# Optimization experiments

Measured on AMD Instinct MI355X. Metric: run time of the kernel, lower is better.

## Reference

```python
import jax, jax.numpy as jnp
import numpy as np
from math import log2, ceil

HEADS, DIM_HEAD, BLOCK, EPS = 16, 64, 16, 1e-8


def setup_inputs() -> dict:
    key = jax.random.key(0)
    k1, k2, k3, k4 = jax.random.split(key, 4)
    b, n, dim = 4, 4096, 1024
    inner = HEADS * DIM_HEAD
    return {
        "x": jax.random.normal(k1, (b, n, dim), jnp.float32),
        "w_qkv": jax.random.normal(k2, (inner * 3, dim), jnp.float32) * 0.02,
        "w_out": jax.random.normal(k3, (dim, inner), jnp.float32) * 0.02,
        "b_out": jax.random.normal(k4, (dim,), jnp.float32) * 0.02,
    }


def reference(x, w_qkv, w_out, b_out):
    b, n, dim = x.shape
    pad_to_len = 2 ** ceil(log2(n))
    if pad_to_len != n:
        x = jnp.pad(x, ((0, 0), (0, pad_to_len - n), (0, 0)))
    qkv = x @ w_qkv.T  # torch Linear (no bias): weight is [out, in]
    q, k, v = jnp.split(qkv, 3, axis=-1)

    def split_heads(t):
        return t.reshape(b, pad_to_len, HEADS, DIM_HEAD).transpose(0, 2, 1, 3).reshape(b * HEADS, pad_to_len, DIM_HEAD)

    q = split_heads(q) * DIM_HEAD ** -0.5
    k = split_heads(k)
    v = split_heads(v)

    num_levels = int(log2(pad_to_len // BLOCK)) - 1
    # hierarchical coarsening: q,k averaged over pairs, v summed over pairs
    qkvs = [(q, k, v)]
    for _ in range(num_levels):
        q = q.reshape(q.shape[0], -1, 2, DIM_HEAD).mean(2)
        k = k.reshape(k.shape[0], -1, 2, DIM_HEAD).mean(2)
        v = v.reshape(v.shape[0], -1, 2, DIM_HEAD).sum(2)
        qkvs.append((q, k, v))

    neg_max = -jnp.finfo(x.dtype).max
    idx = jnp.arange(pad_to_len)
    Ysum = jnp.zeros((b * HEADS, pad_to_len, DIM_HEAD), x.dtype)
    Asum = jnp.zeros((b * HEADS, pad_to_len), x.dtype)

    for lvl, (ql, kl, vl) in enumerate(qkvs):
        B = ql.shape[0]
        nb = ql.shape[1] // BLOCK  # number of blocks at this level
        ql = ql.reshape(B, nb, BLOCK, DIM_HEAD)
        kl = kl.reshape(B, nb, BLOCK, DIM_HEAD)
        vl = vl.reshape(B, nb, BLOCK, DIM_HEAD)
        if lvl == 0:
            # finest level: causal diagonal block attention
            S = jnp.einsum('bnid,bnjd->bnij', ql, kl)
            S = jnp.where(jnp.triu(jnp.ones((BLOCK, BLOCK), bool), 1), neg_max, S)
            S = S - S.max(-1, keepdims=True)
            A = jnp.exp(S)
            y = jnp.einsum('bnij,bnjd->bnid', A, vl).reshape(B, pad_to_len, DIM_HEAD)
            Av = A.sum(-1).reshape(B, pad_to_len)
        else:
            # off-diagonal: second block of each pair attends to first block of pair
            q2 = ql.reshape(B, nb // 2, 2, BLOCK, DIM_HEAD)[:, :, 1]
            k1b = kl.reshape(B, nb // 2, 2, BLOCK, DIM_HEAD)[:, :, 0]  # flip_every_two then take [:,1]
            v1b = vl.reshape(B, nb // 2, 2, BLOCK, DIM_HEAD)[:, :, 0]
            S = jnp.einsum('bnid,bnjd->bnij', q2, k1b)
            S = S - S.max(-1, keepdims=True)
            A = jnp.exp(S)
            y = jnp.einsum('bnij,bnjd->bnid', A, v1b)  # [B, nb/2, BLOCK, d]
            Av = A.sum(-1)
            # zero-pad first block of each pair, flatten blocks back to sequence
            y = jnp.pad(y[:, :, None], ((0, 0), (0, 0), (1, 0), (0, 0), (0, 0))).reshape(B, -1, DIM_HEAD)
            Av = jnp.pad(Av[:, :, None], ((0, 0), (0, 0), (1, 0), (0, 0))).reshape(B, -1)
            # expand coarsened positions to full resolution (consecutive repeats)
            y = jnp.repeat(y, 2 ** lvl, axis=1)
            Av = jnp.repeat(Av, 2 ** lvl, axis=1)
        # causal keep-mask: max original index inside the coarsened key group <= query index
        seq_key = (idx >> lvl << lvl) + (2 ** lvl - 1)
        keep = seq_key <= idx  # at lvl=0 seq_key == idx -> keep all
        Ysum = Ysum + jnp.where(keep[None, :, None], y, 0.0)
        Asum = Asum + jnp.where(keep[None, :], Av, 0.0)

    out = Ysum / (Asum + EPS)[..., None]
    out = out.reshape(b, HEADS, pad_to_len, DIM_HEAD).transpose(0, 2, 1, 3).reshape(b, pad_to_len, HEADS * DIM_HEAD)
    out = out @ w_out.T + b_out
    return out[:, :n]
```

## Files before the change

### kernel.cpp

```cpp
#include <hip/hip_runtime.h>

typedef __bf16 bf16_t;
typedef __attribute__((ext_vector_type(8))) __bf16 bf16x8;
typedef __attribute__((ext_vector_type(4))) float f32x4;

#define MFMA(a,b,c) __builtin_amdgcn_mfma_f32_16x16x32_bf16(a,b,c,0,0,0)

static __device__ __forceinline__ unsigned short f2bfbits(float f){
  unsigned int u = __builtin_bit_cast(unsigned int, f);
  return (unsigned short)((u + 0x7FFFu + ((u >> 16) & 1u)) >> 16);
}
static __device__ __forceinline__ float bits2f(unsigned int b){
  return __builtin_bit_cast(float, b << 16);
}
static __device__ __forceinline__ void gl_lds16(const void* g, void* l){
  __builtin_amdgcn_global_load_lds(
      (const __attribute__((address_space(1))) void*)(g),
      (__attribute__((address_space(3))) void*)(l), 16, 0, 0);
}
static __device__ __forceinline__ void unpack8(uint4 raw, float* f){
  f[0]=bits2f(raw.x&0xFFFFu); f[1]=bits2f(raw.x>>16);
  f[2]=bits2f(raw.y&0xFFFFu); f[3]=bits2f(raw.y>>16);
  f[4]=bits2f(raw.z&0xFFFFu); f[5]=bits2f(raw.z>>16);
  f[6]=bits2f(raw.w&0xFFFFu); f[7]=bits2f(raw.w>>16);
}

__global__ __launch_bounds__(256) void cvt_f32_bf16(const float* __restrict__ in,
                                                    unsigned short* __restrict__ out,
                                                    long n4){
  const long stride = (long)gridDim.x * 256;
  for (long i = (long)blockIdx.x * 256 + threadIdx.x; i < n4; i += stride){
    float4 v = *(const float4*)(in + i * 4);
    unsigned long long pack = (unsigned long long)f2bfbits(v.x)
      | ((unsigned long long)f2bfbits(v.y) << 16)
      | ((unsigned long long)f2bfbits(v.z) << 32)
      | ((unsigned long long)f2bfbits(v.w) << 48);
    *(unsigned long long*)(out + i * 4) = pack;
  }
}

template<int MODE>
__global__ __launch_bounds__(512, 2) void gemm256(
    const unsigned short* __restrict__ A, const unsigned short* __restrict__ B,
    const int K, const int nbx,
    unsigned short* __restrict__ oq, unsigned short* __restrict__ ok2, unsigned short* __restrict__ ov,
    float* __restrict__ outp, const float* __restrict__ bias)
{
  __shared__ char lds[131072];
  const int t = threadIdx.x;
  const int lane = t & 63, wid = t >> 6;
  const int wr = wid >> 2, wc = wid & 3;
  const int r16 = lane & 15, g = lane >> 4;

  const int nb = gridDim.x, cpx = nb >> 3;
  const int lin = (blockIdx.x & 7) * cpx + (blockIdx.x >> 3);
  const int by = lin / nbx, bx = lin - by * nbx;
  const long row0 = (long)by * 256, col0 = (long)bx * 256;

  const unsigned short* gA[4]; const unsigned short* gB[4];
  int ldsoff[4];
  #pragma unroll
  for (int r2 = 0; r2 < 4; ++r2){
    const int flat = r2*512 + t;
    const int row = flat >> 3, slot = flat & 7;
    const int slotg = slot ^ (row & 7);
    gA[r2] = A + (row0 + row) * K + slotg*8;
    gB[r2] = B + (col0 + row) * K + slotg*8;
    ldsoff[r2] = (r2*512 + wid*64) * 16;
  }

  f32x4 acc[8][4];
  #pragma unroll
  for (int m = 0; m < 8; ++m)
    #pragma unroll
    for (int n = 0; n < 4; ++n)
      acc[m][n] = (f32x4){0.f, 0.f, 0.f, 0.f};

  const int nk = K >> 6;

  #pragma unroll
  for (int r2 = 0; r2 < 4; ++r2){
    gl_lds16(gA[r2], lds + ldsoff[r2]);
    gl_lds16(gB[r2], lds + 32768 + ldsoff[r2]);
  }

  for (int kt = 0; kt < nk; ++kt){
    char* ldsA = lds + (kt & 1)*65536;
    char* ldsB = ldsA + 32768;
    if (kt + 1 < nk){
      char* nA = lds + ((kt+1)&1)*65536;
      const int koff = (kt+1)*64;
      #pragma unroll
      for (int r2 = 0; r2 < 4; ++r2){
        gl_lds16(gA[r2] + koff, nA + ldsoff[r2]);
        gl_lds16(gB[r2] + koff, nA + 32768 + ldsoff[r2]);
      }
      asm volatile("s_waitcnt vmcnt(8)" ::: "memory");
    } else {
      asm volatile("s_waitcnt vmcnt(0)" ::: "memory");
    }
    __builtin_amdgcn_s_barrier();
    __builtin_amdgcn_sched_barrier(0);

    bf16x8 bfrag[4][2];
    #pragma unroll
    for (int n = 0; n < 4; ++n)
      #pragma unroll
      for (int kk = 0; kk < 2; ++kk){
        const int row = wc*64 + n*16 + r16;
        bfrag[n][kk] = *(const bf16x8*)(ldsB + row*128 + (((kk*4 + g) ^ (row & 7)) * 16));
      }
    #pragma unroll
    for (int mp = 0; mp < 4; ++mp){
      bf16x8 afr[2][2];
      #pragma unroll
      for (int mi = 0; mi < 2; ++mi)
        #pragma unroll
        for (int kk = 0; kk < 2; ++kk){
          const int row = wr*128 + (mp*2 + mi)*16 + r16;
          afr[mi][kk] = *(const bf16x8*)(ldsA + row*128 + (((kk*4 + g) ^ (row & 7)) * 16));
        }
      __builtin_amdgcn_s_setprio(1);
      #pragma unroll
      for (int mi = 0; mi < 2; ++mi)
        #pragma unroll
        for (int n = 0; n < 4; ++n)
          #pragma unroll
          for (int kk = 0; kk < 2; ++kk)
            acc[mp*2 + mi][n] = MFMA(afr[mi][kk], bfrag[n][kk], acc[mp*2 + mi][n]);
      __builtin_amdgcn_s_setprio(0);
    }
    __builtin_amdgcn_sched_barrier(0);
    __builtin_amdgcn_s_barrier();
  }

  if (MODE == 0){
    __syncthreads();
    const int which = (int)(col0 >> 10);
    const int h = (int)((col0 & 1023) >> 6) + wc;
    const float sc = (which == 0) ? 0.125f : 1.0f;
    unsigned short* st = (unsigned short*)lds + wid*8192;
    #pragma unroll
    for (int pass = 0; pass < 2; ++pass){
      #pragma unroll
      for (int mm = 0; mm < 4; ++mm)
        #pragma unroll
        for (int n = 0; n < 4; ++n)
          #pragma unroll
          for (int q2 = 0; q2 < 4; ++q2)
            st[(mm*16 + g*4 + q2)*72 + n*16 + r16] = f2bfbits(acc[pass*4 + mm][n][q2] * sc);
      const long prow0 = row0 + wr*128 + pass*64;
      if (which < 2){
        unsigned short* dst = (which == 0) ? oq : ok2;
        #pragma unroll
        for (int rd = 0; rd < 8; ++rd){
          const int rl = rd*8 + (lane >> 3);
          const int gr = lane & 7;
          uint4 v = *(const uint4*)&st[rl*72 + gr*8];
          const long ii = prow0 + rl;
          const int b_ = (int)(ii >> 12), pos = (int)(ii & 4095);
          *(uint4*)&dst[(((long)b_*16 + h)*4096 + pos)*64 + gr*8] = v;
        }
      } else {
        #pragma unroll
        for (int rd = 0; rd < 8; ++rd){
          const int blk = rd >> 1;
          const int d = (rd & 1)*32 + (lane >> 1);
          const int kkh = lane & 1;
          unsigned short tmp[8];
          #pragma unroll
          for (int j = 0; j < 8; ++j)
            tmp[j] = st[(blk*16 + kkh*8 + j)*72 + d];
          uint4 v;
          v.x = (unsigned int)tmp[0] | ((unsigned int)tmp[1] << 16);
          v.y = (unsigned int)tmp[2] | ((unsigned int)tmp[3] << 16);
          v.z = (unsigned int)tmp[4] | ((unsigned int)tmp[5] << 16);
          v.w = (unsigned int)tmp[6] | ((unsigned int)tmp[7] << 16);
          const long posblk = (prow0 >> 4) + blk;
          const int b_ = (int)(posblk >> 8), blkg = (int)(posblk & 255);
          *(uint4*)&ov[(((long)b_*16 + h)*256 + blkg)*1024 + d*16 + kkh*8] = v;
        }
      }
      __builtin_amdgcn_sched_barrier(0);
    }
  } else {
    #pragma unroll
    for (int n = 0; n < 4; ++n){
      const long j = col0 + wc*64 + n*16 + r16;
      const float bi = bias[j];
      #pragma unroll
      for (int m = 0; m < 8; ++m){
        const long ib = row0 + wr*128 + m*16 + g*4;
        #pragma unroll
        for (int q2 = 0; q2 < 4; ++q2)
          outp[(ib + q2)*1024 + j] = acc[m][n][q2] + bi;
      }
    }
  }
}

__global__ __launch_bounds__(256) void coarsen(
    const unsigned short* __restrict__ q0, const unsigned short* __restrict__ k0,
    const unsigned short* __restrict__ vt0,
    unsigned short* __restrict__ qch, unsigned short* __restrict__ kch,
    unsigned short* __restrict__ vch)
{
  __shared__ float Abuf[128*64];
  __shared__ float Bbuf[64*64];
  const int t = threadIdx.x;
  const int chunk = blockIdx.x;
  const int bh = blockIdx.y;
  const int arr = blockIdx.z;
  if (arr < 2){
    const unsigned short* src = (arr == 0) ? q0 : k0;
    const long sbase = ((long)bh*4096 + (long)chunk*128) * 64;
    #pragma unroll
    for (int it = 0; it < 4; ++it){
      const int idx = it*2048 + t*8;
      uint4 raw = *(const uint4*)(src + sbase + idx);
      float f[8]; unpack8(raw, f);
      #pragma unroll
      for (int j = 0; j < 8; ++j) Abuf[idx + j] = f[j];
    }
  } else {
    const long sbase = ((long)bh*256 + (long)chunk*8) * 1024;
    #pragma unroll
    for (int it = 0; it < 4; ++it){
      const int flat = it*2048 + t*8;
      const int blk = flat >> 10, rem = flat & 1023;
      const int d = rem >> 4, kk0 = rem & 15;
      uint4 raw = *(const uint4*)(vt0 + sbase + flat);
      float f[8]; unpack8(raw, f);
      #pragma unroll
      for (int j = 0; j < 8; ++j) Abuf[(blk*16 + kk0 + j)*64 + d] = f[j];
    }
  }
  __syncthreads();
  float* cur = Abuf; float* nxt = Bbuf;
  int rows = 128;
  const int Spre[8] = {0, 0, 1024, 1536, 1792, 1920, 1984, 2016};
  for (int l = 1; l <= 7; ++l){
    rows >>= 1;
    const int P = 2048 >> l;
    const long base = (long)Spre[l] * 4096;
    for (int e = t; e < rows*64; e += 256){
      const int p = e >> 6, d = e & 63;
      const float a = cur[(2*p)*64 + d], b2 = cur[(2*p + 1)*64 + d];
      const float val = (arr == 2) ? (a + b2) : 0.5f*(a + b2);
      nxt[e] = val;
      const int pl = chunk*rows + p;
      const int cb = pl >> 4, ci = cb >> 1;
      const unsigned short bv = f2bfbits(val);
      if (arr == 0){
        if (cb & 1) qch[base + ((long)bh*P + ci*16 + (pl & 15))*64 + d] = bv;
      } else if (arr == 1){
        if (!(cb & 1)) kch[base + ((long)bh*P + ci*16 + (pl & 15))*64 + d] = bv;
      } else {
        if (!(cb & 1)) vch[base + (long)bh*P*64 + ci*1024 + d*16 + (pl & 15)] = bv;
      }
    }
    __syncthreads();
    float* tmp = cur; cur = nxt; nxt = tmp;
  }
}

__global__ __launch_bounds__(256) void attn_fused(
    const unsigned short* __restrict__ q0, const unsigned short* __restrict__ k0,
    const unsigned short* __restrict__ vt0,
    const unsigned short* __restrict__ qch, const unsigned short* __restrict__ kch,
    const unsigned short* __restrict__ vch,
    unsigned short* __restrict__ ybf)
{
  const int lane = threadIdx.x & 63;
  const int w = threadIdx.x >> 6;
  const int B0 = blockIdx.x * 4 + w;
  const int bh = blockIdx.y;
  const int b_ = bh >> 4, h = bh & 15;
  const int r = lane & 15, g = lane >> 4;
  __shared__ float accs_all[4][16*64];
  __shared__ float denoms_all[4][16];
  float* accs = accs_all[w];
  float* denoms = denoms_all[w];

  {
    const long base = ((long)bh*4096 + (long)B0*16) * 64;
    const bf16x8 ka0 = *(const bf16x8*)(k0 + base + r*64 + g*8);
    const bf16x8 ka1 = *(const bf16x8*)(k0 + base + r*64 + g*8 + 32);
    const bf16x8 qb0 = *(const bf16x8*)(q0 + base + r*64 + g*8);
    const bf16x8 qb1 = *(const bf16x8*)(q0 + base + r*64 + g*8 + 32);
    f32x4 s = {0.f,0.f,0.f,0.f};
    s = MFMA(ka0, qb0, s);
    s = MFMA(ka1, qb1, s);

    float p[4];
    float mx = -3.402823466e38f;
    #pragma unroll
    for (int j = 0; j < 4; ++j){
      const int c = g*4 + j;
      p[j] = (c <= r) ? s[j] : -3.402823466e38f;
      mx = fmaxf(mx, p[j]);
    }
    mx = fmaxf(mx, __shfl_xor(mx, 16));
    mx = fmaxf(mx, __shfl_xor(mx, 32));
    float rs = 0.f;
    #pragma unroll
    for (int j = 0; j < 4; ++j){
      const int c = g*4 + j;
      p[j] = (c <= r) ? __expf(p[j] - mx) : 0.f;
      rs += p[j];
    }
    rs += __shfl_xor(rs, 16);
    rs += __shfl_xor(rs, 32);

    float x16[4], x32[4], x48[4];
    #pragma unroll
    for (int j = 0; j < 4; ++j){
      x16[j] = __shfl_xor(p[j], 16);
      x32[j] = __shfl_xor(p[j], 32);
      x48[j] = __shfl_xor(p[j], 48);
    }
    bf16x8 af;
    #pragma unroll
    for (int j = 0; j < 4; ++j){
      const float lo = (g == 0) ? p[j]   : (g == 1) ? x48[j] : 0.f;
      const float hi = (g == 0) ? x16[j] : (g == 1) ? x32[j] : 0.f;
      af[j]   = (bf16_t)lo;
      af[j+4] = (bf16_t)hi;
    }
    const unsigned short* vt = vt0 + ((long)bh*256 + B0) * 1024;
    #pragma unroll
    for (int nb = 0; nb < 4; ++nb){
      bf16x8 bv;
      #pragma unroll
      for (int j = 0; j < 8; ++j) bv[j] = (bf16_t)0.f;
      if (g < 2) bv = *(const bf16x8*)(vt + (nb*16 + r)*16 + g*8);
      f32x4 y = {0.f,0.f,0.f,0.f};
      y = MFMA(af, bv, y);
      #pragma unroll
      for (int q2 = 0; q2 < 4; ++q2)
        accs[(g*4 + q2)*64 + nb*16 + r] = y[q2];
    }
    if (g == 0) denoms[r] = rs;
  }

  const int Spre[8] = {0, 0, 1024, 1536, 1792, 1920, 1984, 2016};
  for (int l = 1; l <= 7; ++l){
    int nr, lo, cb;
    if (l <= 4){
      nr = 16 >> l;
      lo = (B0 & ((1 << l) - 1)) << (4 - l);
      cb = B0 >> l;
    } else {
      const int m = 1 << (l - 4);
      if ((B0 & (m - 1)) != m - 1) continue;
      const int qrow = ((B0 + 1) >> (l - 4)) - 1;
      cb = qrow >> 4; lo = qrow & 15; nr = 1;
    }
    if (!(cb & 1)) continue;
    const int ci = cb >> 1;
    const int P = 2048 >> l;
    const long base = (long)Spre[l] * 4096;
    const long qb_base = base + ((long)bh*P + ci*16) * 64;
    const long kv_base = base + (long)bh*P*64 + (long)ci*1024;

    const bf16x8 ka0 = *(const bf16x8*)(kch + qb_base + r*64 + g*8);
    const bf16x8 ka1 = *(const bf16x8*)(kch + qb_base + r*64 + g*8 + 32);
    const bf16x8 qb0 = *(const bf16x8*)(qch + qb_base + r*64 + g*8);
    const bf16x8 qb1 = *(const bf16x8*)(qch + qb_base + r*64 + g*8 + 32);
    f32x4 s = {0.f,0.f,0.f,0.f};
    s = MFMA(ka0, qb0, s);
    s = MFMA(ka1, qb1, s);

    float p[4];
    float mx = fmaxf(fmaxf(s[0], s[1]), fmaxf(s[2], s[3]));
    mx = fmaxf(mx, __shfl_xor(mx, 16));
    mx = fmaxf(mx, __shfl_xor(mx, 32));
    float rs = 0.f;
    #pragma unroll
    for (int j = 0; j < 4; ++j){ p[j] = __expf(s[j] - mx); rs += p[j]; }
    rs += __shfl_xor(rs, 16);
    rs += __shfl_xor(rs, 32);

    float x16[4], x32[4], x48[4];
    #pragma unroll
    for (int j = 0; j < 4; ++j){
      x16[j] = __shfl_xor(p[j], 16);
      x32[j] = __shfl_xor(p[j], 32);
      x48[j] = __shfl_xor(p[j], 48);
    }
    bf16x8 af;
    #pragma unroll
    for (int j = 0; j < 4; ++j){
      const float lo2 = (g == 0) ? p[j]   : (g == 1) ? x48[j] : 0.f;
      const float hi2 = (g == 0) ? x16[j] : (g == 1) ? x32[j] : 0.f;
      af[j]   = (bf16_t)lo2;
      af[j+4] = (bf16_t)hi2;
    }
    #pragma unroll
    for (int nb = 0; nb < 4; ++nb){
      bf16x8 bv;
      #pragma unroll
      for (int j = 0; j < 8; ++j) bv[j] = (bf16_t)0.f;
      if (g < 2) bv = *(const bf16x8*)(vch + kv_base + (nb*16 + r)*16 + g*8);
      f32x4 y = {0.f,0.f,0.f,0.f};
      y = MFMA(af, bv, y);
      #pragma unroll
      for (int q2 = 0; q2 < 4; ++q2){
        const int row = g*4 + q2;
        if (row >= lo && row < lo + nr){
          const int ii = (((cb*16 + row + 1) << l) - 1) - (B0 << 4);
          accs[ii*64 + nb*16 + r] += y[q2];
        }
      }
    }
    if (g == 0 && r >= lo && r < lo + nr){
      const int ii = (((cb*16 + r + 1) << l) - 1) - (B0 << 4);
      denoms[ii] += rs;
    }
  }

  const int row = lane >> 2, d0 = (lane & 3) * 16;
  const float inv = 1.f / (denoms[row] + 1e-8f);
  unsigned int wv[8];
  #pragma unroll
  for (int j2 = 0; j2 < 8; ++j2){
    const float a = accs[row*64 + d0 + 2*j2]      * inv;
    const float b2 = accs[row*64 + d0 + 2*j2 + 1] * inv;
    wv[j2] = (unsigned int)f2bfbits(a) | ((unsigned int)f2bfbits(b2) << 16);
  }
  uint4* dst = (uint4*)(ybf + ((long)b_*4096 + B0*16 + row)*1024 + h*64 + d0);
  dst[0] = make_uint4(wv[0], wv[1], wv[2], wv[3]);
  dst[1] = make_uint4(wv[4], wv[5], wv[6], wv[7]);
}

extern "C" void kernel_launch(void* const* d_in, const int* in_sizes, int n_in,
                              void* d_out, int out_size, void* d_ws, size_t ws_size,
                              hipStream_t stream){
  const float* x    = (const float*)d_in[0];
  const float* wqkv = (const float*)d_in[1];
  const float* wout = (const float*)d_in[2];
  const float* bout = (const float*)d_in[3];
  float* out = (float*)d_out;
  char* ws = (char*)d_ws;

  unsigned short* wqb = (unsigned short*)(ws + 0L);
  unsigned short* wob = (unsigned short*)(ws + 6291456L);
  unsigned short* xb  = (unsigned short*)(ws + 8388608L);
  unsigned short* q0  = (unsigned short*)(ws + 41943040L);
  unsigned short* k0  = (unsigned short*)(ws + 75497472L);
  unsigned short* vt0 = (unsigned short*)(ws + 109051904L);
  unsigned short* qch = (unsigned short*)(ws + 142606336L);
  unsigned short* kch = (unsigned short*)(ws + 159252480L);
  unsigned short* vch = (unsigned short*)(ws + 175898624L);
  unsigned short* ybf = xb;

  cvt_f32_bf16<<<2048, 256, 0, stream>>>(x,    xb,  (long)16384*1024/4);
  cvt_f32_bf16<<<512,  256, 0, stream>>>(wqkv, wqb, (long)3072*1024/4);
  cvt_f32_bf16<<<256,  256, 0, stream>>>(wout, wob, (long)1024*1024/4);

  gemm256<0><<<768, 512, 0, stream>>>(xb, wqb, 1024, 12, q0, k0, vt0, nullptr, nullptr);
  coarsen<<<dim3(32,64,3), 256, 0, stream>>>(q0, k0, vt0, qch, kch, vch);
  attn_fused<<<dim3(64,64), 256, 0, stream>>>(q0, k0, vt0, qch, kch, vch, ybf);
  gemm256<1><<<256, 512, 0, stream>>>(ybf, wob, 1024, 4, nullptr, nullptr, nullptr, out, bout);
}
```

Before: 305.0 us.

## Interleave GEMM prefetch into MFMA sub-stages and pad coarsen LDS buffers

The GEMM main loop is split into four sub-stages, one per pair of A row-tiles. Each sub-stage issues part of the next tile's global-to-LDS loads and uses finer vmcnt/lgkmcnt waits and barriers, so memory traffic overlaps with MFMA work instead of arriving as one burst at the top of each iteration. Separately, the coarsen kernel pads its LDS rows to 65 floats to avoid bank conflicts. It also writes the transposed V output through a second pass that makes the global stores coalesced. The extra barriers per k-step add synchronization overhead and could hurt if the compute phases are short.

```diff
diff --git a/kernel.cpp b/kernel.cpp
--- a/kernel.cpp
+++ b/kernel.cpp
@@ -78,48 +78,39 @@
 
   const int nk = K >> 6;
 
-  #pragma unroll
-  for (int r2 = 0; r2 < 4; ++r2){
-    gl_lds16(gA[r2], lds + ldsoff[r2]);
-    gl_lds16(gB[r2], lds + 32768 + ldsoff[r2]);
-  }
+  #define SA(tt, r) gl_lds16(gA[r] + (tt)*64, lds + ((tt)&1)*65536 + ldsoff[r])
+  #define SB(tt, r) gl_lds16(gB[r] + (tt)*64, lds + ((tt)&1)*65536 + 32768 + ldsoff[r])
+
+  SA(0,0); SA(0,2); SB(0,0); SB(0,1); SB(0,2); SB(0,3); SA(0,1); SA(0,3);
+  asm volatile("s_waitcnt vmcnt(2)" ::: "memory");
+  __builtin_amdgcn_s_barrier();
 
   for (int kt = 0; kt < nk; ++kt){
     char* ldsA = lds + (kt & 1)*65536;
     char* ldsB = ldsA + 32768;
-    if (kt + 1 < nk){
-      char* nA = lds + ((kt+1)&1)*65536;
-      const int koff = (kt+1)*64;
-      #pragma unroll
-      for (int r2 = 0; r2 < 4; ++r2){
-        gl_lds16(gA[r2] + koff, nA + ldsoff[r2]);
-        gl_lds16(gB[r2] + koff, nA + 32768 + ldsoff[r2]);
-      }
-      asm volatile("s_waitcnt vmcnt(8)" ::: "memory");
-    } else {
-      asm volatile("s_waitcnt vmcnt(0)" ::: "memory");
-    }
-    __builtin_amdgcn_s_barrier();
-    __builtin_amdgcn_sched_barrier(0);
-
+    const bool more = (kt + 1 < nk);
     bf16x8 bfrag[4][2];
-    #pragma unroll
-    for (int n = 0; n < 4; ++n)
-      #pragma unroll
-      for (int kk = 0; kk < 2; ++kk){
-        const int row = wc*64 + n*16 + r16;
-        bfrag[n][kk] = *(const bf16x8*)(ldsB + row*128 + (((kk*4 + g) ^ (row & 7)) * 16));
-      }
-    #pragma unroll
-    for (int mp = 0; mp < 4; ++mp){
+
+    {
+      #pragma unroll
+      for (int n = 0; n < 4; ++n)
+        #pragma unroll
+        for (int kk = 0; kk < 2; ++kk){
+          const int row = wc*64 + n*16 + r16;
+          bfrag[n][kk] = *(const bf16x8*)(ldsB + row*128 + (((kk*4 + g) ^ (row & 7)) * 16));
+        }
       bf16x8 afr[2][2];
       #pragma unroll
       for (int mi = 0; mi < 2; ++mi)
         #pragma unroll
         for (int kk = 0; kk < 2; ++kk){
-          const int row = wr*128 + (mp*2 + mi)*16 + r16;
+          const int row = wr*128 + mi*16 + r16;
           afr[mi][kk] = *(const bf16x8*)(ldsA + row*128 + (((kk*4 + g) ^ (row & 7)) * 16));
         }
+      if (more){ SA(kt+1,0); SA(kt+1,2); }
+      __builtin_amdgcn_s_barrier();
+      asm volatile("s_waitcnt lgkmcnt(0)" ::: "memory");
+      __builtin_amdgcn_sched_barrier(0);
       __builtin_amdgcn_s_setprio(1);
       #pragma unroll
       for (int mi = 0; mi < 2; ++mi)
@@ -127,12 +118,93 @@
         for (int n = 0; n < 4; ++n)
           #pragma unroll
           for (int kk = 0; kk < 2; ++kk)
-            acc[mp*2 + mi][n] = MFMA(afr[mi][kk], bfrag[n][kk], acc[mp*2 + mi][n]);
+            acc[mi][n] = MFMA(afr[mi][kk], bfrag[n][kk], acc[mi][n]);
       __builtin_amdgcn_s_setprio(0);
-    }
-    __builtin_amdgcn_sched_barrier(0);
-    __builtin_amdgcn_s_barrier();
-  }
+      __builtin_amdgcn_s_barrier();
+    }
+    {
+      bf16x8 afr[2][2];
+      #pragma unroll
+      for (int mi = 0; mi < 2; ++mi)
+        #pragma unroll
+        for (int kk = 0; kk < 2; ++kk){
+          const int row = wr*128 + (2+mi)*16 + r16;
+          afr[mi][kk] = *(const bf16x8*)(ldsA + row*128 + (((kk*4 + g) ^ (row & 7)) * 16));
+        }
+      if (more){
+        SB(kt+1,0); SB(kt+1,1);
+        asm volatile("s_waitcnt vmcnt(4)" ::: "memory");
+      } else {
+        asm volatile("s_waitcnt vmcnt(0)" ::: "memory");
+      }
+      __builtin_amdgcn_s_barrier();
+      asm volatile("s_waitcnt lgkmcnt(0)" ::: "memory");
+      __builtin_amdgcn_sched_barrier(0);
+      __builtin_amdgcn_s_setprio(1);
+      #pragma unroll
+      for (int mi = 0; mi < 2; ++mi)
+        #pragma unroll
+        for (int n = 0; n < 4; ++n)
+          #pragma unroll
+          for (int kk = 0; kk < 2; ++kk)
+            acc[2+mi][n] = MFMA(afr[mi][kk], bfrag[n][kk], acc[2+mi][n]);
+      __builtin_amdgcn_s_setprio(0);
+      __builtin_amdgcn_s_barrier();
+    }
+    {
+      bf16x8 afr[2][2];
+      #pragma unroll
+      for (int mi = 0; mi < 2; ++mi)
+        #pragma unroll
+        for (int kk = 0; kk < 2; ++kk){
+          const int row = wr*128 + (4+mi)*16 + r16;
+          afr[mi][kk] = *(const bf16x8*)(ldsA + row*128 + (((kk*4 + g) ^ (row & 7)) * 16));
+        }
+      if (more){ SB(kt+1,2); SB(kt+1,3); }
+      __builtin_amdgcn_s_barrier();
+      asm volatile("s_waitcnt lgkmcnt(0)" ::: "memory");
+      __builtin_amdgcn_sched_barrier(0);
+      __builtin_amdgcn_s_setprio(1);
+      #pragma unroll
+      for (int mi = 0; mi < 2; ++mi)
+        #pragma unroll
+        for (int n = 0; n < 4; ++n)
+          #pragma unroll
+          for (int kk = 0; kk < 2; ++kk)
+            acc[4+mi][n] = MFMA(afr[mi][kk], bfrag[n][kk], acc[4+mi][n]);
+      __builtin_amdgcn_s_setprio(0);
+      __builtin_amdgcn_s_barrier();
+    }
+    {
+      bf16x8 afr[2][2];
+      #pragma unroll
+      for (int mi = 0; mi < 2; ++mi)
+        #pragma unroll
+        for (int kk = 0; kk < 2; ++kk){
+          const int row = wr*128 + (6+mi)*16 + r16;
+          afr[mi][kk] = *(const bf16x8*)(ldsA + row*128 + (((kk*4 + g) ^ (row & 7)) * 16));
+        }
+      if (more){
+        SA(kt+1,1); SA(kt+1,3);
+        asm volatile("s_waitcnt vmcnt(2)" ::: "memory");
+      }
+      __builtin_amdgcn_s_barrier();
+      asm volatile("s_waitcnt lgkmcnt(0)" ::: "memory");
+      __builtin_amdgcn_sched_barrier(0);
+      __builtin_amdgcn_s_setprio(1);
+      #pragma unroll
+      for (int mi = 0; mi < 2; ++mi)
+        #pragma unroll
+        for (int n = 0; n < 4; ++n)
+          #pragma unroll
+          for (int kk = 0; kk < 2; ++kk)
+            acc[6+mi][n] = MFMA(afr[mi][kk], bfrag[n][kk], acc[6+mi][n]);
+      __builtin_amdgcn_s_setprio(0);
+      __builtin_amdgcn_s_barrier();
+    }
+  }
+  #undef SA
+  #undef SB
 
   if (MODE == 0){
     __syncthreads();
@@ -205,8 +277,8 @@
     unsigned short* __restrict__ qch, unsigned short* __restrict__ kch,
     unsigned short* __restrict__ vch)
 {
-  __shared__ float Abuf[128*64];
-  __shared__ float Bbuf[64*64];
+  __shared__ float Abuf[128*65];
+  __shared__ float Bbuf[64*65];
   const int t = threadIdx.x;
   const int chunk = blockIdx.x;
   const int bh = blockIdx.y;
@@ -219,8 +291,9 @@
       const int idx = it*2048 + t*8;
       uint4 raw = *(const uint4*)(src + sbase + idx);
       float f[8]; unpack8(raw, f);
-      #pragma unroll
-      for (int j = 0; j < 8; ++j) Abuf[idx + j] = f[j];
+      const int rowb = idx >> 6, colb = idx & 63;
+      #pragma unroll
+      for (int j = 0; j < 8; ++j) Abuf[rowb*65 + colb + j] = f[j];
     }
   } else {
     const long sbase = ((long)bh*256 + (long)chunk*8) * 1024;
@@ -232,7 +305,7 @@
       uint4 raw = *(const uint4*)(vt0 + sbase + flat);
       float f[8]; unpack8(raw, f);
       #pragma unroll
-      for (int j = 0; j < 8; ++j) Abuf[(blk*16 + kk0 + j)*64 + d] = f[j];
+      for (int j = 0; j < 8; ++j) Abuf[(blk*16 + kk0 + j)*65 + d] = f[j];
     }
   }
   __syncthreads();
@@ -245,21 +318,30 @@
     const long base = (long)Spre[l] * 4096;
     for (int e = t; e < rows*64; e += 256){
       const int p = e >> 6, d = e & 63;
-      const float a = cur[(2*p)*64 + d], b2 = cur[(2*p + 1)*64 + d];
+      const float a = cur[(2*p)*65 + d], b2 = cur[(2*p + 1)*65 + d];
       const float val = (arr == 2) ? (a + b2) : 0.5f*(a + b2);
-      nxt[e] = val;
+      nxt[p*65 + d] = val;
       const int pl = chunk*rows + p;
       const int cb = pl >> 4, ci = cb >> 1;
-      const unsigned short bv = f2bfbits(val);
       if (arr == 0){
-        if (cb & 1) qch[base + ((long)bh*P + ci*16 + (pl & 15))*64 + d] = bv;
+        if (cb & 1) qch[base + ((long)bh*P + ci*16 + (pl & 15))*64 + d] = f2bfbits(val);
       } else if (arr == 1){
-        if (!(cb & 1)) kch[base + ((long)bh*P + ci*16 + (pl & 15))*64 + d] = bv;
-      } else {
-        if (!(cb & 1)) vch[base + (long)bh*P*64 + ci*1024 + d*16 + (pl & 15)] = bv;
+        if (!(cb & 1)) kch[base + ((long)bh*P + ci*16 + (pl & 15))*64 + d] = f2bfbits(val);
+      } else if (rows < 16){
+        if (!(cb & 1)) vch[base + (long)bh*P*64 + ci*1024 + d*16 + (pl & 15)] = f2bfbits(val);
       }
     }
     __syncthreads();
+    if (arr == 2 && rows >= 16){
+      const int nblk = rows >> 4;
+      for (int oe = t; oe < nblk*1024; oe += 256){
+        const int bl = oe >> 10, rem = oe & 1023;
+        const int cb = chunk*nblk + bl;
+        if (cb & 1) continue;
+        const int d = rem >> 4, kk = rem & 15;
+        vch[base + (long)bh*P*64 + (long)(cb>>1)*1024 + rem] = f2bfbits(nxt[(bl*16 + kk)*65 + d]);
+      }
+    }
     float* tmp = cur; cur = nxt; nxt = tmp;
   }
 }
```

New measurement: 306.6 us. No clear change (+0.5%).
